# Optimization experiments

Measured on AMD Instinct MI355X. Metric: run time of the kernel, lower is better.

## Reference

```python
import jax, jax.numpy as jnp
import numpy as np

N_COLS = 4096
N_ROWS = 4096
H = 64          # args.hidden1
S = 2           # per-edge supp feature count (cv_supp/vc_supp dim 0)
S_VO = 2        # vo_supp feature dim
S_CO = 2        # co_supp feature dim
EDGE_DENSITY = 0.03


def setup_inputs() -> dict:
    key = jax.random.key(0)
    ks = jax.random.split(key, 20)
    col_hidden = jax.random.normal(ks[0], (N_COLS, H), jnp.float32)
    row_hidden = jax.random.normal(ks[1], (N_ROWS, H), jnp.float32)
    obj_hidden = jax.random.normal(ks[2], (1, H), jnp.float32)
    # sparse bipartite adjacency encoded in supp[0] != 0 (as in the TF code)
    mask = jax.random.bernoulli(ks[3], EDGE_DENSITY, (N_ROWS, N_COLS))
    cv_supp = jax.random.normal(ks[4], (S, N_ROWS, N_COLS), jnp.float32) * mask[None]
    vc_supp = jnp.transpose(cv_supp, (0, 2, 1))  # [S, ncols, nrows]
    vo_supp = jax.random.normal(ks[5], (N_COLS, S_VO), jnp.float32)
    co_supp = jax.random.normal(ks[6], (N_ROWS, S_CO), jnp.float32)
    w = 0.05
    W_vo = jax.random.normal(ks[7], (2 * H, H), jnp.float32) * w
    W_oc = jax.random.normal(ks[8], (2 * H, H), jnp.float32) * w
    W_vc = jax.random.normal(ks[9], (2 * H, H), jnp.float32) * w
    W_co = jax.random.normal(ks[10], (2 * H, H), jnp.float32) * w
    W_ov = jax.random.normal(ks[11], (2 * H, H), jnp.float32) * w
    W_cv = jax.random.normal(ks[12], (2 * H, H), jnp.float32) * w
    # attention scorer nets: Dense(concat_dim -> 1) + sigmoid
    w_attn_vo = jax.random.normal(ks[13], (2 * H + S_VO, 1), jnp.float32) * 0.1
    b_attn_vo = jnp.zeros((), jnp.float32)
    w_attn_co = jax.random.normal(ks[14], (2 * H + S_CO, 1), jnp.float32) * 0.1
    b_attn_co = jnp.zeros((), jnp.float32)
    # pairwise attn nets decomposed into [col | supp | row] weight slices
    w_cv_col = jax.random.normal(ks[15], (H,), jnp.float32) * 0.1
    w_cv_supp = jax.random.normal(ks[16], (S,), jnp.float32) * 0.1
    w_cv_row = jax.random.normal(ks[17], (H,), jnp.float32) * 0.1
    b_cv = jnp.zeros((), jnp.float32)
    w_vc_row = jax.random.normal(ks[18], (H,), jnp.float32) * 0.1
    w_vc_supp = jax.random.normal(ks[19], (S,), jnp.float32) * 0.1
    w_vc_col = jax.random.normal(jax.random.fold_in(key, 99), (H,), jnp.float32) * 0.1
    b_vc = jnp.zeros((), jnp.float32)
    return dict(col_hidden=col_hidden, row_hidden=row_hidden, obj_hidden=obj_hidden,
                cv_supp=cv_supp, vc_supp=vc_supp, vo_supp=vo_supp, co_supp=co_supp,
                W_vo=W_vo, W_oc=W_oc, W_vc=W_vc, W_co=W_co, W_ov=W_ov, W_cv=W_cv,
                w_attn_vo=w_attn_vo, b_attn_vo=b_attn_vo,
                w_attn_co=w_attn_co, b_attn_co=b_attn_co,
                w_cv_col=w_cv_col, w_cv_supp=w_cv_supp, w_cv_row=w_cv_row, b_cv=b_cv,
                w_vc_row=w_vc_row, w_vc_supp=w_vc_supp, w_vc_col=w_vc_col, b_vc=b_vc)


def _forward(col_hidden, row_hidden, obj_hidden, cv_supp, vc_supp, vo_supp, co_supp,
             W_vo, W_oc, W_vc, W_co, W_ov, W_cv,
             w_attn_vo, b_attn_vo, w_attn_co, b_attn_co,
             w_cv_col, w_cv_supp, w_cv_row, b_cv,
             w_vc_row, w_vc_supp, w_vc_col, b_vc):
    act = jax.nn.relu
    ncols, nrows = col_hidden.shape[0], row_hidden.shape[0]
    # ---- v -> o: attend over all columns, update obj node ----
    vo_in = jnp.concatenate([col_hidden, vo_supp,
                             jnp.broadcast_to(obj_hidden, (ncols, H))], axis=1)
    a_vo = jax.nn.sigmoid(vo_in @ w_attn_vo + b_attn_vo)          # [ncols, 1]
    v_o_out = a_vo.T @ col_hidden                                  # [1, H]
    obj = act(jnp.concatenate([obj_hidden, v_o_out], axis=1) @ W_vo)
    # ---- v -> c: per-row ragged neighbor attention, vectorized via masked pairwise scores ----
    nbr_cv = cv_supp[0] != 0                                       # [nrows, ncols]
    logits_cv = ((row_hidden @ w_cv_row)[:, None]
                 + (col_hidden @ w_cv_col)[None, :]
                 + jnp.einsum('snc,s->nc', cv_supp, w_cv_supp) + b_cv)
    score_cv = jnp.where(nbr_cv, jax.nn.sigmoid(logits_cv), 0.0)   # [nrows, ncols]
    v_out = score_cv @ col_hidden                                  # [nrows, H]
    o_c_out = act(jnp.concatenate([jnp.broadcast_to(obj, (nrows, H)), row_hidden], axis=1) @ W_oc)
    row_next = act(jnp.concatenate([o_c_out, v_out], axis=1) @ W_vc)
    # ---- c -> o ----
    co_in = jnp.concatenate([row_next, co_supp,
                             jnp.broadcast_to(obj, (nrows, H))], axis=1)
    a_co = jax.nn.sigmoid(co_in @ w_attn_co + b_attn_co)           # [nrows, 1]
    c_o_out = a_co.T @ row_next                                    # [1, H]
    obj = act(jnp.concatenate([obj, c_o_out], axis=1) @ W_co)
    # ---- c -> v ----
    nbr_vc = vc_supp[0] != 0                                       # [ncols, nrows]
    logits_vc = ((col_hidden @ w_vc_col)[:, None]
                 + (row_next @ w_vc_row)[None, :]
                 + jnp.einsum('scn,s->cn', vc_supp, w_vc_supp) + b_vc)
    score_vc = jnp.where(nbr_vc, jax.nn.sigmoid(logits_vc), 0.0)   # [ncols, nrows]
    c_out = score_vc @ row_next                                    # [ncols, H]
    o_v_out = act(jnp.concatenate([jnp.broadcast_to(obj, (ncols, H)), col_hidden], axis=1) @ W_ov)
    col_next = act(jnp.concatenate([o_v_out, c_out], axis=1) @ W_cv)
    return col_next, row_next, obj


def reference(col_hidden, row_hidden, obj_hidden, cv_supp, vc_supp, vo_supp, co_supp,
              W_vo, W_oc, W_vc, W_co, W_ov, W_cv,
              w_attn_vo, b_attn_vo, w_attn_co, b_attn_co,
              w_cv_col, w_cv_supp, w_cv_row, b_cv,
              w_vc_row, w_vc_supp, w_vc_col, b_vc):
    col_next, row_next, obj = _forward(
        col_hidden, row_hidden, obj_hidden, cv_supp, vc_supp, vo_supp, co_supp,
        W_vo, W_oc, W_vc, W_co, W_ov, W_cv,
        w_attn_vo, b_attn_vo, w_attn_co, b_attn_co,
        w_cv_col, w_cv_supp, w_cv_row, b_cv,
        w_vc_row, w_vc_supp, w_vc_col, b_vc)
    # original layer also passes the supp tensors through unchanged
    return (col_next, row_next, obj, cv_supp, vc_supp, vo_supp, co_supp)
```

## Files before the change

kernel.cpp:

```cpp
#include <hip/hip_runtime.h>
#include <math.h>

typedef float f4 __attribute__((ext_vector_type(4)));

#define PLANE (4096*4096)

#define OUT_COL 0
#define OUT_ROW 262144
#define OUT_OBJ 524288
#define OUT_CV  524352
#define OUT_VC  34078784
#define OUT_VO  67633216
#define OUT_CO  67641408

#define WS_VO_P 0
#define WS_CO_P 4096
#define WS_OBJ1 8192
#define WS_RDCV 8256
#define WS_CDCV 12352
#define WS_RDVC 16448
#define WS_CDVC 20544
#define WS_PART 24640

__device__ __forceinline__ float sigf(float x) {
    return 1.0f / (1.0f + __expf(-x));
}

#define AS1 __attribute__((address_space(1)))
#define AS3 __attribute__((address_space(3)))
__device__ __forceinline__ void gl_lds16(const float* g, float* l) {
    __builtin_amdgcn_global_load_lds((const AS1 void*)g, (AS3 void*)l, 16, 0, 0);
}

__device__ __forceinline__ void attn_body64(
    int blk, int t, const float* __restrict__ X, const float* __restrict__ supp,
    const float* __restrict__ obj, const float* __restrict__ wat,
    const float* __restrict__ bat, float* __restrict__ accP,
    const float* __restrict__ wextra, float* __restrict__ dextra,
    float* sA, float* sAcc)
{
    const int w = t >> 6, lane = t & 63;
    if (t < 64) {
        const int i = blk * 64 + t;
        float od = 0.f;
        for (int h = 0; h < 64; ++h) od += obj[h] * wat[66 + h];
        float x = bat[0] + od + supp[i*2] * wat[64] + supp[i*2+1] * wat[65];
        const f4* Xr = (const f4*)(X + i*64);
        f4 xd = 0.f, dd = 0.f;
        #pragma unroll
        for (int q = 0; q < 16; ++q) {
            f4 xv = Xr[q];
            xd += xv * ((const f4*)wat)[q];
            if (wextra) dd += xv * ((const f4*)wextra)[q];
        }
        x += xd.x + xd.y + xd.z + xd.w;
        if (dextra) dextra[i] = dd.x + dd.y + dd.z + dd.w;
        sA[t] = sigf(x);
        sAcc[t] = 0.f;
    }
    __syncthreads();
    float partial = 0.f;
    const int jbase = blk * 64 + w * 16;
    for (int j = 0; j < 16; ++j)
        partial += sA[w*16 + j] * X[(jbase + j)*64 + lane];
    atomicAdd(&sAcc[lane], partial);
    __syncthreads();
    if (t < 64) accP[blk*64 + t] = sAcc[t];
}

__global__ __launch_bounds__(256) void k_front(
    const float* __restrict__ col_hidden, const float* __restrict__ row_hidden,
    const float* __restrict__ w_cv_col, const float* __restrict__ w_vc_col,
    const float* __restrict__ w_cv_row,
    float* __restrict__ cdcv, float* __restrict__ cdvc, float* __restrict__ rdcv,
    const float* __restrict__ vo_supp, const float* __restrict__ co_supp,
    float* __restrict__ out_vo, float* __restrict__ out_co,
    const float* __restrict__ obj_hidden, const float* __restrict__ w_attn_vo,
    const float* __restrict__ b_attn_vo, float* __restrict__ voP)
{
    __shared__ float sA[64];
    __shared__ float sAcc[64];
    const int t = threadIdx.x;
    if (blockIdx.x < 3072) {
        const int gw = blockIdx.x * 4 + (t >> 6);
        const int lane = t & 63;
        const int which = gw >> 12;
        const int row = gw & 4095;
        const float* x; const float* w; float* dst;
        if (which == 0)      { x = col_hidden; w = w_cv_col; dst = cdcv; }
        else if (which == 1) { x = col_hidden; w = w_vc_col; dst = cdvc; }
        else                 { x = row_hidden; w = w_cv_row; dst = rdcv; }
        float v = x[row * 64 + lane] * w[lane];
        #pragma unroll
        for (int off = 32; off; off >>= 1) v += __shfl_down(v, off, 64);
        if (lane == 0) dst[row] = v;
        return;
    }
    if (blockIdx.x < 3088) {
        const int idx = (blockIdx.x - 3072) * 256 + t;
        if (idx < 2048) ((f4*)out_vo)[idx] = ((const f4*)vo_supp)[idx];
        else            ((f4*)out_co)[idx - 2048] = ((const f4*)co_supp)[idx - 2048];
        return;
    }
    attn_body64(blockIdx.x - 3088, t, col_hidden, vo_supp, obj_hidden,
                w_attn_vo, b_attn_vo, voP, nullptr, nullptr, sA, sAcc);
}

__global__ __launch_bounds__(256) void k_attn(
    const float* __restrict__ X, const float* __restrict__ supp,
    const float* __restrict__ obj, const float* __restrict__ wat,
    const float* __restrict__ bat, float* __restrict__ accP,
    const float* __restrict__ wextra, float* __restrict__ dextra)
{
    __shared__ float sA[64];
    __shared__ float sAcc[64];
    attn_body64(blockIdx.x, threadIdx.x, X, supp, obj, wat, bat, accP,
                wextra, dextra, sA, sAcc);
}

__global__ __launch_bounds__(512, 2) void k_big(
    const float* __restrict__ supp0, const float* __restrict__ supp1,
    const float* __restrict__ Bm,
    const float* __restrict__ rdot, const float* __restrict__ cdot,
    const float* __restrict__ wsup, const float* __restrict__ bias,
    float* __restrict__ part, float* __restrict__ pass0, float* __restrict__ pass1,
    const float* __restrict__ objL, const float* __restrict__ objRp,
    const float* __restrict__ Wobj, float* __restrict__ objDst)
{
    __shared__ __align__(16) float lds[2][2][8192];
    const int t = threadIdx.x;

    if (blockIdx.x == 256) {
        if (t < 64) {
            float r = 0.f;
            for (int b = 0; b < 64; ++b) r += objRp[b*64 + t];
            lds[0][0][t] = r;
        }
        __syncthreads();
        if (t < 64) {
            float acc = 0.f;
            for (int k = 0; k < 64; ++k) acc += objL[k] * Wobj[k*64 + t];
            for (int k = 0; k < 64; ++k) acc += lds[0][0][k] * Wobj[(64+k)*64 + t];
            objDst[t] = fmaxf(acc, 0.f);
        }
        return;
    }

    const int bi = blockIdx.x >> 2;
    const int jg = blockIdx.x & 3;
    const int i0 = bi * 64;
    const int w = t >> 6, lane = t & 63;
    const float w0 = wsup[0], w1 = wsup[1], bv = bias[0];
    const bool producer = (w >= 4);
    const int pw = w & 3;

    for (int it = 0; it <= 8; ++it) {
        if (producer && it < 8) {
            float* s0 = &lds[it & 1][0][0];
            float* s1 = &lds[it & 1][1][0];
            const int jt0 = (jg * 8 + it) * 128;
            for (int k = 0; k < 8; ++k) {
                const int p = pw + 4 * k;
                const size_t g = (size_t)(i0 + 2*p + (lane >> 5)) * 4096 + jt0 + (lane & 31) * 4;
                gl_lds16(supp0 + g, s0 + p * 256);
                gl_lds16(supp1 + g, s1 + p * 256);
            }
            asm volatile("s_waitcnt vmcnt(0)" ::: "memory");
            __builtin_amdgcn_sched_barrier(0);
            const int c4 = (lane & 31) * 4;
            const f4 cd = *(const f4*)(cdot + jt0 + c4);
            for (int q = 0; q < 8; ++q) {
                const int p = q * 4 + pw;
                const int row = 2 * p + (lane >> 5);
                f4 a0 = *(const f4*)(s0 + row * 128 + c4);
                f4 a1 = *(const f4*)(s1 + row * 128 + c4);
                const size_t g = (size_t)(i0 + row) * 4096 + jt0 + c4;
                *(f4*)(pass0 + g) = a0;
                *(f4*)(pass1 + g) = a1;
                const float rd = rdot[i0 + row];
                f4 lg = rd + cd + w0*a0 + w1*a1 + bv;
                f4 s;
                s.x = (a0.x != 0.f) ? sigf(lg.x) : 0.f;
                s.y = (a0.y != 0.f) ? sigf(lg.y) : 0.f;
                s.z = (a0.z != 0.f) ? sigf(lg.z) : 0.f;
                s.w = (a0.w != 0.f) ? sigf(lg.w) : 0.f;
                const int swz = (lane & 31) ^ (((row >> 2) & 3) << 1);
                *(f4*)(s0 + row * 128 + swz * 4) = s;
            }
            asm volatile("s_waitcnt lgkmcnt(0)" ::: "memory");
            __builtin_amdgcn_sched_barrier(0);
            for (int k = 0; k < 8; ++k) {
                const int c = pw + 4 * k;
                gl_lds16(Bm + (size_t)(jt0 + c * 4) * 64 + lane * 4, s1 + c * 256);
            }
        } else if (!producer && it >= 1) {
            const float* s0 = &lds[(it - 1) & 1][0][0];
            const float* s1 = &lds[(it - 1) & 1][1][0];
            const int ilb = t >> 4;
            const int hf4 = t & 15;
            const int sw  = (ilb & 3) << 1;
            f4 acc0 = 0.f, acc1 = 0.f, acc2 = 0.f, acc3 = 0.f;
            #pragma unroll 4
            for (int jf = 0; jf < 32; ++jf) {
                const int jj = jf * 4;
                f4 b0 = *(const f4*)(s1 + (jj + 0) * 64 + hf4 * 4);
                f4 b1 = *(const f4*)(s1 + (jj + 1) * 64 + hf4 * 4);
                f4 b2 = *(const f4*)(s1 + (jj + 2) * 64 + hf4 * 4);
                f4 b3 = *(const f4*)(s1 + (jj + 3) * 64 + hf4 * 4);
                const int sf = (jf ^ sw) * 4;
                { f4 s = *(const f4*)(s0 + (ilb*4 + 0) * 128 + sf); acc0 += s.x*b0 + s.y*b1 + s.z*b2 + s.w*b3; }
                { f4 s = *(const f4*)(s0 + (ilb*4 + 1) * 128 + sf); acc1 += s.x*b0 + s.y*b1 + s.z*b2 + s.w*b3; }
                { f4 s = *(const f4*)(s0 + (ilb*4 + 2) * 128 + sf); acc2 += s.x*b0 + s.y*b1 + s.z*b2 + s.w*b3; }
                { f4 s = *(const f4*)(s0 + (ilb*4 + 3) * 128 + sf); acc3 += s.x*b0 + s.y*b1 + s.z*b2 + s.w*b3; }
            }
            const int js = jg * 8 + (it - 1);
            float* pb = part + (size_t)js * 262144 + (size_t)i0 * 64;
            *(f4*)(pb + (ilb*4 + 0)*64 + hf4*4) = acc0;
            *(f4*)(pb + (ilb*4 + 1)*64 + hf4*4) = acc1;
            *(f4*)(pb + (ilb*4 + 2)*64 + hf4*4) = acc2;
            *(f4*)(pb + (ilb*4 + 3)*64 + hf4*4) = acc3;
        }
        __syncthreads();
    }
}

__global__ __launch_bounds__(256) void k_mlp2(
    const float* __restrict__ objx, const float* __restrict__ base,
    const float* __restrict__ W1, const float* __restrict__ part,
    const float* __restrict__ W2, float* __restrict__ dst)
{
    __shared__ float mid[4][64];
    __shared__ float accsP[4][256];
    __shared__ float accs[4][64];
    const int t = threadIdx.x, w = t >> 6, h = t & 63, lane = t & 63;
    const int nbase = blockIdx.x * 4;
    f4 v = 0.f;
    for (int j = w; j < 32; j += 4)
        v += *(const f4*)(part + (size_t)j * 262144 + blockIdx.x * 256 + lane * 4);
    *(f4*)&accsP[w][lane * 4] = v;
    float m = 0.f;
    for (int k = 0; k < 64; ++k) m += objx[k] * W1[k*64 + h];
    for (int k = 0; k < 64; ++k) m += base[(nbase + w)*64 + k] * W1[(64+k)*64 + h];
    mid[w][h] = fmaxf(m, 0.f);
    __syncthreads();
    accs[t >> 6][t & 63] = accsP[0][t] + accsP[1][t] + accsP[2][t] + accsP[3][t];
    __syncthreads();
    float o = 0.f;
    for (int k = 0; k < 64; ++k) o += mid[w][k] * W2[k*64 + h];
    for (int k = 0; k < 64; ++k) o += accs[w][k] * W2[(64+k)*64 + h];
    dst[(nbase + w)*64 + h] = fmaxf(o, 0.f);
}

extern "C" void kernel_launch(void* const* d_in, const int* in_sizes, int n_in,
                              void* d_out, int out_size, void* d_ws, size_t ws_size,
                              hipStream_t stream)
{
    const float* col_hidden = (const float*)d_in[0];
    const float* row_hidden = (const float*)d_in[1];
    const float* obj_hidden = (const float*)d_in[2];
    const float* cv_supp    = (const float*)d_in[3];
    const float* vc_supp    = (const float*)d_in[4];
    const float* vo_supp    = (const float*)d_in[5];
    const float* co_supp    = (const float*)d_in[6];
    const float* W_vo       = (const float*)d_in[7];
    const float* W_oc       = (const float*)d_in[8];
    const float* W_vc       = (const float*)d_in[9];
    const float* W_co       = (const float*)d_in[10];
    const float* W_ov       = (const float*)d_in[11];
    const float* W_cv       = (const float*)d_in[12];
    const float* w_attn_vo  = (const float*)d_in[13];
    const float* b_attn_vo  = (const float*)d_in[14];
    const float* w_attn_co  = (const float*)d_in[15];
    const float* b_attn_co  = (const float*)d_in[16];
    const float* w_cv_col   = (const float*)d_in[17];
    const float* w_cv_supp  = (const float*)d_in[18];
    const float* w_cv_row   = (const float*)d_in[19];
    const float* b_cv       = (const float*)d_in[20];
    const float* w_vc_row   = (const float*)d_in[21];
    const float* w_vc_supp  = (const float*)d_in[22];
    const float* w_vc_col   = (const float*)d_in[23];
    const float* b_vc       = (const float*)d_in[24];

    float* out = (float*)d_out;
    float* ws  = (float*)d_ws;

    k_front<<<3152, 256, 0, stream>>>(col_hidden, row_hidden, w_cv_col, w_vc_col, w_cv_row,
                                      ws + WS_CDCV, ws + WS_CDVC, ws + WS_RDCV,
                                      vo_supp, co_supp, out + OUT_VO, out + OUT_CO,
                                      obj_hidden, w_attn_vo, b_attn_vo, ws + WS_VO_P);
    k_big<<<257, 512, 0, stream>>>(cv_supp, cv_supp + PLANE, col_hidden,
                                   ws + WS_RDCV, ws + WS_CDCV, w_cv_supp, b_cv,
                                   ws + WS_PART, out + OUT_CV, out + OUT_CV + PLANE,
                                   obj_hidden, ws + WS_VO_P, W_vo, ws + WS_OBJ1);
    k_mlp2<<<1024, 256, 0, stream>>>(ws + WS_OBJ1, row_hidden, W_oc, ws + WS_PART, W_vc,
                                     out + OUT_ROW);
    k_attn<<<64, 256, 0, stream>>>(out + OUT_ROW, co_supp, ws + WS_OBJ1, w_attn_co, b_attn_co,
                                   ws + WS_CO_P, w_vc_row, ws + WS_RDVC);
    k_big<<<257, 512, 0, stream>>>(vc_supp, vc_supp + PLANE, out + OUT_ROW,
                                   ws + WS_CDVC, ws + WS_RDVC, w_vc_supp, b_vc,
                                   ws + WS_PART, out + OUT_VC, out + OUT_VC + PLANE,
                                   ws + WS_OBJ1, ws + WS_CO_P, W_co, out + OUT_OBJ);
    k_mlp2<<<1024, 256, 0, stream>>>(out + OUT_OBJ, col_hidden, W_ov, ws + WS_PART, W_cv,
                                     out + OUT_COL);
}
```

Before: 585.8 us.

## Replace dense tile matmul in k_big with compacted sparse-edge gather accumulation

Each 64x128 tile now compacts the nonzero edges of every row into LDS using a warp prefix-scan. Each sigmoid score is stored with its column index packed into the low 8 mantissa bits. Each row's H-dimension accumulation then loops only over its nonzero edges and gathers the matching B rows from global memory, instead of running a dense 128-wide product. The producer/consumer double-buffered pipeline is dropped in favour of many small independent blocks (2049 x 256 threads). The aim is to skip the dense FP32 FMA work, which is mostly multiplying by zeros at this edge density. The costs are slightly reduced score precision, a cap of 126 nonzeros per row chunk, and irregular gathers from global memory.

```diff
diff --git a/kernel.cpp b/kernel.cpp
--- a/kernel.cpp
+++ b/kernel.cpp
@@ -30,6 +30,16 @@
 #define AS3 __attribute__((address_space(3)))
 __device__ __forceinline__ void gl_lds16(const float* g, float* l) {
     __builtin_amdgcn_global_load_lds((const AS1 void*)g, (AS3 void*)l, 16, 0, 0);
+}
+
+#define LGKM_BARRIER do { \
+    asm volatile("s_waitcnt lgkmcnt(0)" ::: "memory"); \
+    __builtin_amdgcn_sched_barrier(0); \
+    __builtin_amdgcn_s_barrier(); \
+    __builtin_amdgcn_sched_barrier(0); } while (0)
+
+__device__ __forceinline__ float enc_sj(float s, int j) {
+    return __uint_as_float((__float_as_uint(s) & 0xFFFFFF00u) | (unsigned)j);
 }
 
 __device__ __forceinline__ void attn_body64(
@@ -118,7 +128,7 @@
                 wextra, dextra, sA, sAcc);
 }
 
-__global__ __launch_bounds__(512, 2) void k_big(
+__global__ __launch_bounds__(256, 2) void k_big(
     const float* __restrict__ supp0, const float* __restrict__ supp1,
     const float* __restrict__ Bm,
     const float* __restrict__ rdot, const float* __restrict__ cdot,
@@ -127,100 +137,97 @@
     const float* __restrict__ objL, const float* __restrict__ objRp,
     const float* __restrict__ Wobj, float* __restrict__ objDst)
 {
-    __shared__ __align__(16) float lds[2][2][8192];
+    __shared__ __align__(16) float lds0[64*128];
+    __shared__ __align__(16) float lds1[64*128];
     const int t = threadIdx.x;
 
-    if (blockIdx.x == 256) {
+    if (blockIdx.x == 2048) {
         if (t < 64) {
             float r = 0.f;
             for (int b = 0; b < 64; ++b) r += objRp[b*64 + t];
-            lds[0][0][t] = r;
+            lds0[t] = r;
         }
         __syncthreads();
         if (t < 64) {
             float acc = 0.f;
             for (int k = 0; k < 64; ++k) acc += objL[k] * Wobj[k*64 + t];
-            for (int k = 0; k < 64; ++k) acc += lds[0][0][k] * Wobj[(64+k)*64 + t];
+            for (int k = 0; k < 64; ++k) acc += lds0[k] * Wobj[(64+k)*64 + t];
             objDst[t] = fmaxf(acc, 0.f);
         }
         return;
     }
 
-    const int bi = blockIdx.x >> 2;
-    const int jg = blockIdx.x & 3;
+    const int bi = blockIdx.x >> 5;
+    const int bj = blockIdx.x & 31;
     const int i0 = bi * 64;
+    const int jt0 = bj * 128;
     const int w = t >> 6, lane = t & 63;
     const float w0 = wsup[0], w1 = wsup[1], bv = bias[0];
-    const bool producer = (w >= 4);
-    const int pw = w & 3;
-
-    for (int it = 0; it <= 8; ++it) {
-        if (producer && it < 8) {
-            float* s0 = &lds[it & 1][0][0];
-            float* s1 = &lds[it & 1][1][0];
-            const int jt0 = (jg * 8 + it) * 128;
-            for (int k = 0; k < 8; ++k) {
-                const int p = pw + 4 * k;
-                const size_t g = (size_t)(i0 + 2*p + (lane >> 5)) * 4096 + jt0 + (lane & 31) * 4;
-                gl_lds16(supp0 + g, s0 + p * 256);
-                gl_lds16(supp1 + g, s1 + p * 256);
+
+    for (int k = 0; k < 8; ++k) {
+        const int p = w * 8 + k;
+        const size_t g = (size_t)(i0 + 2*p + (lane >> 5)) * 4096 + jt0 + (lane & 31) * 4;
+        gl_lds16(supp0 + g, lds0 + p * 256);
+        gl_lds16(supp1 + g, lds1 + p * 256);
+    }
+    __syncthreads();
+
+    {
+        const int hi  = lane >> 5;
+        const int f4c = lane & 31;
+        const int sl  = lane & 31;
+        const f4 cd = *(const f4*)(cdot + jt0 + f4c * 4);
+        for (int q = 0; q < 8; ++q) {
+            const int p = q * 4 + w;
+            const int row = 2 * p + hi;
+            f4 a0 = *(const f4*)(lds0 + row * 128 + f4c * 4);
+            f4 a1 = *(const f4*)(lds1 + row * 128 + f4c * 4);
+            const size_t g = (size_t)(i0 + row) * 4096 + jt0 + f4c * 4;
+            *(f4*)(pass0 + g) = a0;
+            *(f4*)(pass1 + g) = a1;
+            const float rd = rdot[i0 + row];
+            f4 lg = rd + cd + w0 * a0 + w1 * a1 + bv;
+            const int c0 = (a0.x != 0.f), c1 = (a0.y != 0.f);
+            const int c2 = (a0.z != 0.f), c3 = (a0.w != 0.f);
+            const int m = c0 + c1 + c2 + c3;
+            int sum = m;
+            #pragma unroll
+            for (int d = 1; d < 32; d <<= 1) {
+                int x = __shfl_up(sum, d, 32);
+                if (sl >= d) sum += x;
             }
-            asm volatile("s_waitcnt vmcnt(0)" ::: "memory");
-            __builtin_amdgcn_sched_barrier(0);
-            const int c4 = (lane & 31) * 4;
-            const f4 cd = *(const f4*)(cdot + jt0 + c4);
-            for (int q = 0; q < 8; ++q) {
-                const int p = q * 4 + pw;
-                const int row = 2 * p + (lane >> 5);
-                f4 a0 = *(const f4*)(s0 + row * 128 + c4);
-                f4 a1 = *(const f4*)(s1 + row * 128 + c4);
-                const size_t g = (size_t)(i0 + row) * 4096 + jt0 + c4;
-                *(f4*)(pass0 + g) = a0;
-                *(f4*)(pass1 + g) = a1;
-                const float rd = rdot[i0 + row];
-                f4 lg = rd + cd + w0*a0 + w1*a1 + bv;
-                f4 s;
-                s.x = (a0.x != 0.f) ? sigf(lg.x) : 0.f;
-                s.y = (a0.y != 0.f) ? sigf(lg.y) : 0.f;
-                s.z = (a0.z != 0.f) ? sigf(lg.z) : 0.f;
-                s.w = (a0.w != 0.f) ? sigf(lg.w) : 0.f;
-                const int swz = (lane & 31) ^ (((row >> 2) & 3) << 1);
-                *(f4*)(s0 + row * 128 + swz * 4) = s;
-            }
-            asm volatile("s_waitcnt lgkmcnt(0)" ::: "memory");
-            __builtin_amdgcn_sched_barrier(0);
-            for (int k = 0; k < 8; ++k) {
-                const int c = pw + 4 * k;
-                gl_lds16(Bm + (size_t)(jt0 + c * 4) * 64 + lane * 4, s1 + c * 256);
-            }
-        } else if (!producer && it >= 1) {
-            const float* s0 = &lds[(it - 1) & 1][0][0];
-            const float* s1 = &lds[(it - 1) & 1][1][0];
-            const int ilb = t >> 4;
-            const int hf4 = t & 15;
-            const int sw  = (ilb & 3) << 1;
-            f4 acc0 = 0.f, acc1 = 0.f, acc2 = 0.f, acc3 = 0.f;
-            #pragma unroll 4
-            for (int jf = 0; jf < 32; ++jf) {
-                const int jj = jf * 4;
-                f4 b0 = *(const f4*)(s1 + (jj + 0) * 64 + hf4 * 4);
-                f4 b1 = *(const f4*)(s1 + (jj + 1) * 64 + hf4 * 4);
-                f4 b2 = *(const f4*)(s1 + (jj + 2) * 64 + hf4 * 4);
-                f4 b3 = *(const f4*)(s1 + (jj + 3) * 64 + hf4 * 4);
-                const int sf = (jf ^ sw) * 4;
-                { f4 s = *(const f4*)(s0 + (ilb*4 + 0) * 128 + sf); acc0 += s.x*b0 + s.y*b1 + s.z*b2 + s.w*b3; }
-                { f4 s = *(const f4*)(s0 + (ilb*4 + 1) * 128 + sf); acc1 += s.x*b0 + s.y*b1 + s.z*b2 + s.w*b3; }
-                { f4 s = *(const f4*)(s0 + (ilb*4 + 2) * 128 + sf); acc2 += s.x*b0 + s.y*b1 + s.z*b2 + s.w*b3; }
-                { f4 s = *(const f4*)(s0 + (ilb*4 + 3) * 128 + sf); acc3 += s.x*b0 + s.y*b1 + s.z*b2 + s.w*b3; }
-            }
-            const int js = jg * 8 + (it - 1);
-            float* pb = part + (size_t)js * 262144 + (size_t)i0 * 64;
-            *(f4*)(pb + (ilb*4 + 0)*64 + hf4*4) = acc0;
-            *(f4*)(pb + (ilb*4 + 1)*64 + hf4*4) = acc1;
-            *(f4*)(pb + (ilb*4 + 2)*64 + hf4*4) = acc2;
-            *(f4*)(pb + (ilb*4 + 3)*64 + hf4*4) = acc3;
-        }
-        __syncthreads();
+            int pos = sum - m;
+            float* Lrow = lds1 + row * 128;
+            if (c0) { if (pos < 126) Lrow[pos] = enc_sj(sigf(lg.x), f4c*4 + 0); ++pos; }
+            if (c1) { if (pos < 126) Lrow[pos] = enc_sj(sigf(lg.y), f4c*4 + 1); ++pos; }
+            if (c2) { if (pos < 126) Lrow[pos] = enc_sj(sigf(lg.z), f4c*4 + 2); ++pos; }
+            if (c3) { if (pos < 126) Lrow[pos] = enc_sj(sigf(lg.w), f4c*4 + 3); ++pos; }
+            if (sl == 31) Lrow[127] = __int_as_float(sum < 126 ? sum : 126);
+        }
+    }
+    LGKM_BARRIER;
+
+    {
+        const int row = t >> 2;
+        const int hq  = t & 3;
+        const float* Lrow = lds1 + row * 128;
+        const int n = __float_as_int(Lrow[127]);
+        f4 acc0 = 0.f, acc1 = 0.f, acc2 = 0.f, acc3 = 0.f;
+        for (int k = 0; k < n; ++k) {
+            const unsigned u = __float_as_uint(Lrow[k]);
+            const int j = (int)(u & 0xFFu);
+            const float s = __uint_as_float(u & 0xFFFFFF00u);
+            const f4* Br = (const f4*)(Bm + (size_t)(jt0 + j) * 64 + hq * 16);
+            acc0 += s * Br[0];
+            acc1 += s * Br[1];
+            acc2 += s * Br[2];
+            acc3 += s * Br[3];
+        }
+        float* pb = part + (size_t)bj * 262144 + (size_t)(i0 + row) * 64 + hq * 16;
+        *(f4*)(pb + 0)  = acc0;
+        *(f4*)(pb + 4)  = acc1;
+        *(f4*)(pb + 8)  = acc2;
+        *(f4*)(pb + 12) = acc3;
     }
 }
 
@@ -235,6 +242,7 @@
     const int t = threadIdx.x, w = t >> 6, h = t & 63, lane = t & 63;
     const int nbase = blockIdx.x * 4;
     f4 v = 0.f;
+    #pragma unroll
     for (int j = w; j < 32; j += 4)
         v += *(const f4*)(part + (size_t)j * 262144 + blockIdx.x * 256 + lane * 4);
     *(f4*)&accsP[w][lane * 4] = v;
@@ -288,18 +296,18 @@
                                       ws + WS_CDCV, ws + WS_CDVC, ws + WS_RDCV,
                                       vo_supp, co_supp, out + OUT_VO, out + OUT_CO,
                                       obj_hidden, w_attn_vo, b_attn_vo, ws + WS_VO_P);
-    k_big<<<257, 512, 0, stream>>>(cv_supp, cv_supp + PLANE, col_hidden,
-                                   ws + WS_RDCV, ws + WS_CDCV, w_cv_supp, b_cv,
-                                   ws + WS_PART, out + OUT_CV, out + OUT_CV + PLANE,
-                                   obj_hidden, ws + WS_VO_P, W_vo, ws + WS_OBJ1);
+    k_big<<<2049, 256, 0, stream>>>(cv_supp, cv_supp + PLANE, col_hidden,
+                                    ws + WS_RDCV, ws + WS_CDCV, w_cv_supp, b_cv,
+                                    ws + WS_PART, out + OUT_CV, out + OUT_CV + PLANE,
+                                    obj_hidden, ws + WS_VO_P, W_vo, ws + WS_OBJ1);
     k_mlp2<<<1024, 256, 0, stream>>>(ws + WS_OBJ1, row_hidden, W_oc, ws + WS_PART, W_vc,
                                      out + OUT_ROW);
     k_attn<<<64, 256, 0, stream>>>(out + OUT_ROW, co_supp, ws + WS_OBJ1, w_attn_co, b_attn_co,
                                    ws + WS_CO_P, w_vc_row, ws + WS_RDVC);
-    k_big<<<257, 512, 0, stream>>>(vc_supp, vc_supp + PLANE, out + OUT_ROW,
-                                   ws + WS_CDVC, ws + WS_RDVC, w_vc_supp, b_vc,
-                                   ws + WS_PART, out + OUT_VC, out + OUT_VC + PLANE,
-                                   ws + WS_OBJ1, ws + WS_CO_P, W_co, out + OUT_OBJ);
+    k_big<<<2049, 256, 0, stream>>>(vc_supp, vc_supp + PLANE, out + OUT_ROW,
+                                    ws + WS_CDVC, ws + WS_RDVC, w_vc_supp, b_vc,
+                                    ws + WS_PART, out + OUT_VC, out + OUT_VC + PLANE,
+                                    ws + WS_OBJ1, ws + WS_CO_P, W_co, out + OUT_OBJ);
     k_mlp2<<<1024, 256, 0, stream>>>(out + OUT_OBJ, col_hidden, W_ov, ws + WS_PART, W_cv,
                                      out + OUT_COL);
 }
```

Measured after the change: 566.9 us. 1.03x faster.
